# Kernel optimization log

Measured on AMD Instinct MI355X. Metric: run time of the kernel, lower is better.

## Reference

```python
import jax, jax.numpy as jnp
import numpy as np

NEG_SLOPE = 0.2
EPS = 1e-16


def gat_conv(x, src, dst, W, a_src, a_dst, bias, heads, out_ch, n_nodes):
    # x: [N, in], W: [in, heads*out_ch], a_src/a_dst: [heads, out_ch]
    h = (x @ W).reshape(n_nodes, heads, out_ch)            # [N,H,C]
    s_src = jnp.sum(h * a_src[None], axis=-1)              # [N,H]
    s_dst = jnp.sum(h * a_dst[None], axis=-1)              # [N,H]
    e = jax.nn.leaky_relu(s_src[src] + s_dst[dst], NEG_SLOPE)  # [E,H]
    # segment softmax over incoming edges of each destination node
    m = jax.ops.segment_max(e, dst, num_segments=n_nodes)  # [N,H]
    e = jnp.exp(e - m[dst])
    z = jax.ops.segment_sum(e, dst, num_segments=n_nodes)  # [N,H]
    alpha = e / (z[dst] + EPS)                             # [E,H]
    msg = h[src] * alpha[:, :, None]                       # [E,H,C]
    out = jax.ops.segment_sum(msg, dst, num_segments=n_nodes)
    return out.reshape(n_nodes, heads * out_ch) + bias


def setup_inputs() -> dict:
    key = jax.random.key(0)
    ks = jax.random.split(key, 12)
    N, E, D_IN, HID, HEADS, OUT = 100000, 1600000, 16, 128, 8, 3
    C1 = HID // HEADS  # 16 per head
    glorot = lambda k, shape: jax.random.normal(k, shape, jnp.float32) * np.sqrt(2.0 / (shape[0] + shape[-1]))
    return {
        "feature": jax.random.normal(ks[0], (N, D_IN), jnp.float32),
        "edge_index": jax.random.randint(ks[1], (2, E), 0, N, jnp.int64),
        "edge_type": jax.random.randint(ks[2], (E,), 0, 2, jnp.int64),
        "W1": glorot(ks[3], (D_IN, HEADS * C1)),
        "a_src1": glorot(ks[4], (HEADS, C1)),
        "a_dst1": glorot(ks[5], (HEADS, C1)),
        "b1": jnp.zeros((HID,), jnp.float32),
        "W2": glorot(ks[6], (HID, OUT)),
        "a_src2": glorot(ks[7], (1, OUT)),
        "a_dst2": glorot(ks[8], (1, OUT)),
        "b2": jnp.zeros((OUT,), jnp.float32),
    }


def reference(feature, edge_index, edge_type, W1, a_src1, a_dst1, b1, W2, a_src2, a_dst2, b2):
    N = feature.shape[0]
    # PyG GATConv adds self-loops by default
    loop = jnp.arange(N, dtype=edge_index.dtype)
    src = jnp.concatenate([edge_index[0], loop])
    dst = jnp.concatenate([edge_index[1], loop])
    x = gat_conv(feature, src, dst, W1, a_src1, a_dst1, b1, heads=8, out_ch=16, n_nodes=N)
    x = jax.nn.relu(x)
    # dropout is identity in eval mode
    x = gat_conv(x, src, dst, W2, a_src2, a_dst2, b2, heads=1, out_ch=3, n_nodes=N)
    return x
```

## Files before the change

kernel.cpp:

```cpp
#include <hip/hip_runtime.h>
#include <hip/hip_bf16.h>
#include <hip/hip_fp16.h>
#include <math.h>

#define NEG_SLOPE 0.2f
#define GAT_EPS 1e-16f
#define NBB_MAX 128
#define CAP   19456

__global__ __launch_bounds__(1024) void k_part(
    const int* __restrict__ ei, int E, int N, int NB,
    int* __restrict__ cnt, unsigned int* __restrict__ bp)
{
    __shared__ int hist[NBB_MAX];
    __shared__ int base[NBB_MAX];
    int t = threadIdx.x;
    int e0 = blockIdx.x * 4096;
    int srcs[4], dsts[4];
#pragma unroll
    for (int k = 0; k < 4; ++k) {
        int e = e0 + k * 1024 + t;
        if (e < E + N) {
            if (e < E) { srcs[k] = ei[e]; dsts[k] = ei[E + e]; }
            else       { srcs[k] = dsts[k] = e - E; }
        } else dsts[k] = -1;
    }
    if (t < NB) hist[t] = 0;
    __syncthreads();
#pragma unroll
    for (int k = 0; k < 4; ++k)
        if (dsts[k] >= 0) atomicAdd(&hist[dsts[k] >> 10], 1);
    __syncthreads();
    if (t < NB) {
        int c = hist[t];
        base[t] = (c > 0) ? atomicAdd(&cnt[t], c) : 0;
        hist[t] = 0;
    }
    __syncthreads();
#pragma unroll
    for (int k = 0; k < 4; ++k) {
        if (dsts[k] >= 0) {
            int b = dsts[k] >> 10;
            int r = base[b] + atomicAdd(&hist[b], 1);
            if (r < CAP)
                bp[(size_t)b * CAP + r] =
                    ((unsigned)(dsts[k] & 1023) << 17) | (unsigned)srcs[k];
        }
    }
}

__global__ __launch_bounds__(1024) void k_csrgemm(
    const unsigned int* __restrict__ bp, const int* __restrict__ cnt,
    int* __restrict__ offs, int* __restrict__ ends, int* __restrict__ csr,
    int N, int NB,
    const float* __restrict__ x, const float* __restrict__ W1,
    const float* __restrict__ a_src, const float* __restrict__ a_dst,
    __half* __restrict__ h1, float* __restrict__ s_src, float* __restrict__ s_dst)
{
    __shared__ int dcount[1024];
    __shared__ int dtmp[1024];
    __shared__ int doff[1024];
    int t = threadIdx.x;
    if (blockIdx.x >= NB) {
        int gid = (blockIdx.x - NB) * 1024 + t;
        int n = gid >> 5;
        int j4 = gid & 31;
        if (n >= N) return;
        const float4* xr = (const float4*)(x + (size_t)n * 16);
        float4 x0 = xr[0], x1 = xr[1], x2 = xr[2], x3 = xr[3];
        float xs[16] = { x0.x,x0.y,x0.z,x0.w, x1.x,x1.y,x1.z,x1.w,
                         x2.x,x2.y,x2.z,x2.w, x3.x,x3.y,x3.z,x3.w };
        const float4* W4 = (const float4*)W1;
        float4 acc = {0.f, 0.f, 0.f, 0.f};
#pragma unroll
        for (int k = 0; k < 16; ++k) {
            float4 w = W4[k * 32 + j4];
            acc.x += xs[k] * w.x;
            acc.y += xs[k] * w.y;
            acc.z += xs[k] * w.z;
            acc.w += xs[k] * w.w;
        }
        union { __half2 h2v[2]; uint2 u; } pk;
        pk.h2v[0] = __floats2half2_rn(acc.x, acc.y);
        pk.h2v[1] = __floats2half2_rn(acc.z, acc.w);
        ((uint2*)h1)[(size_t)n * 32 + j4] = pk.u;
        float4 av = ((const float4*)a_src)[j4];
        float4 dv = ((const float4*)a_dst)[j4];
        float ps = acc.x*av.x + acc.y*av.y + acc.z*av.z + acc.w*av.w;
        float pd = acc.x*dv.x + acc.y*dv.y + acc.z*dv.z + acc.w*dv.w;
        ps += __shfl_xor(ps, 1); ps += __shfl_xor(ps, 2);
        pd += __shfl_xor(pd, 1); pd += __shfl_xor(pd, 2);
        if ((j4 & 3) == 0) {
            int h = j4 >> 2;
            s_src[n * 8 + h] = ps;
            s_dst[n * 8 + h] = pd;
        }
        return;
    }
    int b = blockIdx.x;
    int rb = b * CAP;
    int m = cnt[b]; if (m > CAP) m = CAP;
    dcount[t] = 0;
    __syncthreads();
    for (int i = t; i < m; i += 1024)
        atomicAdd(&dcount[bp[rb + i] >> 17], 1);
    __syncthreads();
    int v = dcount[t];
    dtmp[t] = v;
    __syncthreads();
    for (int off = 1; off < 1024; off <<= 1) {
        int add = (t >= off) ? dtmp[t - off] : 0;
        __syncthreads();
        dtmp[t] += add;
        __syncthreads();
    }
    doff[t] = dtmp[t] - v;
    int n = b * 1024 + t;
    if (n < N) { offs[n] = rb + doff[t]; ends[n] = rb + dtmp[t]; }
    dcount[t] = 0;
    __syncthreads();
    for (int i = t; i < m; i += 1024) {
        unsigned int p = bp[rb + i];
        int dl = p >> 17;
        int r = atomicAdd(&dcount[dl], 1);
        csr[rb + doff[dl] + r] = (int)(p & 0x1FFFFu);
    }
}

__global__ __launch_bounds__(256) void k_agg1(
    const __half* __restrict__ h1, const float* __restrict__ s_src,
    const float* __restrict__ s_dst, const float* __restrict__ b1,
    const float* __restrict__ W2, const float* __restrict__ a_src2,
    const float* __restrict__ a_dst2,
    const int* __restrict__ offs, const int* __restrict__ ends,
    const int* __restrict__ csr_src,
    float4* __restrict__ h2packed, float* __restrict__ s2d, int N)
{
    int gid = blockIdx.x * 256 + threadIdx.x;
    if (gid >= N * 16) return;
    int n = gid >> 4;
    int t = gid & 15;
    int h = t & 7;
    int half = t >> 3;
    int beg = offs[n], end = ends[n];
    float sd = s_dst[n * 8 + h];

    float z = 0.f;
    float acc[16];
#pragma unroll
    for (int c = 0; c < 16; ++c) acc[c] = 0.f;

    union U { float4 f; __half2 hh[4]; };
    int i = beg + half;
    for (; i + 2 < end; i += 4) {
        int sA = csr_src[i];
        int sB = csr_src[i + 2];
        const float4* hA = (const float4*)(h1 + (size_t)sA * 128 + h * 16);
        const float4* hB = (const float4*)(h1 + (size_t)sB * 128 + h * 16);
        U a0, a1, b0, b1v;
        a0.f = hA[0]; a1.f = hA[1];
        b0.f = hB[0]; b1v.f = hB[1];
        float eA = s_src[sA * 8 + h] + sd;
        float eB = s_src[sB * 8 + h] + sd;
        eA = (eA > 0.f) ? eA : NEG_SLOPE * eA;
        eB = (eB > 0.f) ? eB : NEG_SLOPE * eB;
        float pA = __expf(eA);
        float pB = __expf(eB);
        z += pA + pB;
#pragma unroll
        for (int k = 0; k < 4; ++k) {
            float2 vA = __half22float2(a0.hh[k]);
            float2 vB = __half22float2(b0.hh[k]);
            acc[2 * k]     += pA * vA.x + pB * vB.x;
            acc[2 * k + 1] += pA * vA.y + pB * vB.y;
        }
#pragma unroll
        for (int k = 0; k < 4; ++k) {
            float2 vA = __half22float2(a1.hh[k]);
            float2 vB = __half22float2(b1v.hh[k]);
            acc[8 + 2 * k] += pA * vA.x + pB * vB.x;
            acc[9 + 2 * k] += pA * vA.y + pB * vB.y;
        }
    }
    if (i < end) {
        int sA = csr_src[i];
        const float4* hA = (const float4*)(h1 + (size_t)sA * 128 + h * 16);
        U a0, a1;
        a0.f = hA[0]; a1.f = hA[1];
        float eA = s_src[sA * 8 + h] + sd;
        eA = (eA > 0.f) ? eA : NEG_SLOPE * eA;
        float pA = __expf(eA);
        z += pA;
#pragma unroll
        for (int k = 0; k < 4; ++k) {
            float2 vA = __half22float2(a0.hh[k]);
            acc[2 * k]     += pA * vA.x;
            acc[2 * k + 1] += pA * vA.y;
        }
#pragma unroll
        for (int k = 0; k < 4; ++k) {
            float2 vA = __half22float2(a1.hh[k]);
            acc[8 + 2 * k] += pA * vA.x;
            acc[9 + 2 * k] += pA * vA.y;
        }
    }

    z += __shfl_xor(z, 8);
#pragma unroll
    for (int c = 0; c < 16; ++c) acc[c] += __shfl_xor(acc[c], 8);

    float inv = 1.f / (z + GAT_EPS);

    float r0 = 0.f, r1 = 0.f, r2 = 0.f;
    const float* bb = b1 + h * 16;
    const float* w2 = W2 + h * 16 * 3;
#pragma unroll
    for (int c = 0; c < 16; ++c) {
        float xc = fmaxf(acc[c] * inv + bb[c], 0.f);
        r0 += xc * w2[c * 3 + 0];
        r1 += xc * w2[c * 3 + 1];
        r2 += xc * w2[c * 3 + 2];
    }
#pragma unroll
    for (int m = 4; m >= 1; m >>= 1) {
        r0 += __shfl_xor(r0, m);
        r1 += __shfl_xor(r1, m);
        r2 += __shfl_xor(r2, m);
    }
    if (t == 0) {
        float ss = r0 * a_src2[0] + r1 * a_src2[1] + r2 * a_src2[2];
        float dd = r0 * a_dst2[0] + r1 * a_dst2[1] + r2 * a_dst2[2];
        float4 pk = { r0, r1, r2, ss };
        h2packed[n] = pk;
        s2d[n] = dd;
    }
}

__global__ __launch_bounds__(256) void k_agg2(
    const float4* __restrict__ h2packed, const float* __restrict__ s2d,
    const float* __restrict__ b2,
    const int* __restrict__ offs, const int* __restrict__ ends,
    const int* __restrict__ csr_src,
    float* __restrict__ out, int N)
{
    int gid = blockIdx.x * 256 + threadIdx.x;
    if (gid >= N * 8) return;
    int n = gid >> 3;
    int t = gid & 7;
    int beg = offs[n], end = ends[n];
    float sd = s2d[n];
    float z = 0.f, a0 = 0.f, a1 = 0.f, a2 = 0.f;
    for (int i = beg + t; i < end; i += 8) {
        int src = csr_src[i];
        float4 v = h2packed[src];
        float s = v.w + sd;
        s = (s > 0.f) ? s : NEG_SLOPE * s;
        float p = __expf(s);
        z += p;
        a0 += p * v.x; a1 += p * v.y; a2 += p * v.z;
    }
#pragma unroll
    for (int m = 4; m >= 1; m >>= 1) {
        z  += __shfl_xor(z, m);
        a0 += __shfl_xor(a0, m);
        a1 += __shfl_xor(a1, m);
        a2 += __shfl_xor(a2, m);
    }
    if (t == 0) {
        float inv = 1.f / (z + GAT_EPS);
        out[(size_t)n * 3 + 0] = a0 * inv + b2[0];
        out[(size_t)n * 3 + 1] = a1 * inv + b2[1];
        out[(size_t)n * 3 + 2] = a2 * inv + b2[2];
    }
}

extern "C" void kernel_launch(void* const* d_in, const int* in_sizes, int n_in,
                              void* d_out, int out_size, void* d_ws, size_t ws_size,
                              hipStream_t stream)
{
    const float* feature = (const float*)d_in[0];
    const int*   ei      = (const int*)d_in[1];
    const float* W1      = (const float*)d_in[3];
    const float* a_src1  = (const float*)d_in[4];
    const float* a_dst1  = (const float*)d_in[5];
    const float* b1      = (const float*)d_in[6];
    const float* W2      = (const float*)d_in[7];
    const float* a_src2  = (const float*)d_in[8];
    const float* a_dst2  = (const float*)d_in[9];
    const float* b2      = (const float*)d_in[10];

    const int N = in_sizes[0] / 16;
    const int E = in_sizes[1] / 2;
    const int ET = E + N;
    const int NB = (N + 1023) >> 10;

    char* p = (char*)d_ws;
    auto alloc = [&](size_t bytes) -> void* {
        void* r = (void*)p;
        p += (bytes + 255) & ~(size_t)255;
        return r;
    };
    __half* h1   = (__half*)alloc((size_t)N * 128 * 2);
    float*  s1s  = (float*)alloc((size_t)N * 8 * 4);
    float*  s1d  = (float*)alloc((size_t)N * 8 * 4);
    float4* h2pk = (float4*)alloc((size_t)N * 16);
    float*  s2dv = (float*)alloc((size_t)N * 4);
    int*    offs = (int*)alloc((size_t)N * 4);
    int*    ends = (int*)alloc((size_t)N * 4);
    int*    csr  = (int*)alloc((size_t)NB * CAP * 4);
    unsigned int* bp = (unsigned int*)alloc((size_t)NB * CAP * 4);
    int*    cnt  = (int*)alloc((size_t)NBB_MAX * 4);

    hipMemsetAsync(cnt, 0, (size_t)NB * 4, stream);

    int G2 = (ET + 4095) / 4096;
    k_part<<<G2, 1024, 0, stream>>>(ei, E, N, NB, cnt, bp);

    int G1 = (N * 32 + 1023) / 1024;
    k_csrgemm<<<NB + G1, 1024, 0, stream>>>(
        bp, cnt, offs, ends, csr, N, NB,
        feature, W1, a_src1, a_dst1, h1, s1s, s1d);

    k_agg1<<<(N * 16 + 255) / 256, 256, 0, stream>>>(
        h1, s1s, s1d, b1, W2, a_src2, a_dst2, offs, ends, csr, h2pk, s2dv, N);

    k_agg2<<<(N * 8 + 255) / 256, 256, 0, stream>>>(
        h2pk, s2dv, b2, offs, ends, csr, (float*)d_out, N);
}
```

Before: 168.8 us.

## Split layer-1 GEMM across partition and CSR kernels; unroll aggregation by four

```diff
diff --git a/kernel.cpp b/kernel.cpp
--- a/kernel.cpp
+++ b/kernel.cpp
@@ -8,13 +8,61 @@
 #define NBB_MAX 128
 #define CAP   19456
 
-__global__ __launch_bounds__(1024) void k_part(
-    const int* __restrict__ ei, int E, int N, int NB,
-    int* __restrict__ cnt, unsigned int* __restrict__ bp)
+__device__ __forceinline__ void gemm1_path(
+    int gid, int N,
+    const float* __restrict__ x, const float* __restrict__ W1,
+    const float* __restrict__ a_src, const float* __restrict__ a_dst,
+    __half* __restrict__ h1, float* __restrict__ s_src, float* __restrict__ s_dst)
+{
+    int n = gid >> 5;
+    int j4 = gid & 31;
+    if (n >= N) return;
+    const float4* xr = (const float4*)(x + (size_t)n * 16);
+    float4 x0 = xr[0], x1 = xr[1], x2 = xr[2], x3 = xr[3];
+    float xs[16] = { x0.x,x0.y,x0.z,x0.w, x1.x,x1.y,x1.z,x1.w,
+                     x2.x,x2.y,x2.z,x2.w, x3.x,x3.y,x3.z,x3.w };
+    const float4* W4 = (const float4*)W1;
+    float4 acc = {0.f, 0.f, 0.f, 0.f};
+#pragma unroll
+    for (int k = 0; k < 16; ++k) {
+        float4 w = W4[k * 32 + j4];
+        acc.x += xs[k] * w.x;
+        acc.y += xs[k] * w.y;
+        acc.z += xs[k] * w.z;
+        acc.w += xs[k] * w.w;
+    }
+    union { __half2 h2v[2]; uint2 u; } pk;
+    pk.h2v[0] = __floats2half2_rn(acc.x, acc.y);
+    pk.h2v[1] = __floats2half2_rn(acc.z, acc.w);
+    ((uint2*)h1)[(size_t)n * 32 + j4] = pk.u;
+    float4 av = ((const float4*)a_src)[j4];
+    float4 dv = ((const float4*)a_dst)[j4];
+    float ps = acc.x*av.x + acc.y*av.y + acc.z*av.z + acc.w*av.w;
+    float pd = acc.x*dv.x + acc.y*dv.y + acc.z*dv.z + acc.w*dv.w;
+    ps += __shfl_xor(ps, 1); ps += __shfl_xor(ps, 2);
+    pd += __shfl_xor(pd, 1); pd += __shfl_xor(pd, 2);
+    if ((j4 & 3) == 0) {
+        int h = j4 >> 2;
+        s_src[n * 8 + h] = ps;
+        s_dst[n * 8 + h] = pd;
+    }
+}
+
+__global__ __launch_bounds__(1024) void k_partgemm(
+    const int* __restrict__ ei, int E, int N, int NB, int G2,
+    int* __restrict__ cnt, unsigned int* __restrict__ bp,
+    const float* __restrict__ x, const float* __restrict__ W1,
+    const float* __restrict__ a_src, const float* __restrict__ a_dst,
+    __half* __restrict__ h1, float* __restrict__ s_src, float* __restrict__ s_dst)
 {
     __shared__ int hist[NBB_MAX];
     __shared__ int base[NBB_MAX];
     int t = threadIdx.x;
+    if (blockIdx.x >= G2) {
+        gemm1_path((blockIdx.x - G2) * 1024 + t, N,
+                   x, W1, a_src, a_dst, h1, s_src, s_dst);
+        return;
+    }
     int e0 = blockIdx.x * 4096;
     int srcs[4], dsts[4];
 #pragma unroll
@@ -52,7 +100,7 @@
 __global__ __launch_bounds__(1024) void k_csrgemm(
     const unsigned int* __restrict__ bp, const int* __restrict__ cnt,
     int* __restrict__ offs, int* __restrict__ ends, int* __restrict__ csr,
-    int N, int NB,
+    int N, int NB, int gemmOff,
     const float* __restrict__ x, const float* __restrict__ W1,
     const float* __restrict__ a_src, const float* __restrict__ a_dst,
     __half* __restrict__ h1, float* __restrict__ s_src, float* __restrict__ s_dst)
@@ -62,39 +110,8 @@
     __shared__ int doff[1024];
     int t = threadIdx.x;
     if (blockIdx.x >= NB) {
-        int gid = (blockIdx.x - NB) * 1024 + t;
-        int n = gid >> 5;
-        int j4 = gid & 31;
-        if (n >= N) return;
-        const float4* xr = (const float4*)(x + (size_t)n * 16);
-        float4 x0 = xr[0], x1 = xr[1], x2 = xr[2], x3 = xr[3];
-        float xs[16] = { x0.x,x0.y,x0.z,x0.w, x1.x,x1.y,x1.z,x1.w,
-                         x2.x,x2.y,x2.z,x2.w, x3.x,x3.y,x3.z,x3.w };
-        const float4* W4 = (const float4*)W1;
-        float4 acc = {0.f, 0.f, 0.f, 0.f};
-#pragma unroll
-        for (int k = 0; k < 16; ++k) {
-            float4 w = W4[k * 32 + j4];
-            acc.x += xs[k] * w.x;
-            acc.y += xs[k] * w.y;
-            acc.z += xs[k] * w.z;
-            acc.w += xs[k] * w.w;
-        }
-        union { __half2 h2v[2]; uint2 u; } pk;
-        pk.h2v[0] = __floats2half2_rn(acc.x, acc.y);
-        pk.h2v[1] = __floats2half2_rn(acc.z, acc.w);
-        ((uint2*)h1)[(size_t)n * 32 + j4] = pk.u;
-        float4 av = ((const float4*)a_src)[j4];
-        float4 dv = ((const float4*)a_dst)[j4];
-        float ps = acc.x*av.x + acc.y*av.y + acc.z*av.z + acc.w*av.w;
-        float pd = acc.x*dv.x + acc.y*dv.y + acc.z*dv.z + acc.w*dv.w;
-        ps += __shfl_xor(ps, 1); ps += __shfl_xor(ps, 2);
-        pd += __shfl_xor(pd, 1); pd += __shfl_xor(pd, 2);
-        if ((j4 & 3) == 0) {
-            int h = j4 >> 2;
-            s_src[n * 8 + h] = ps;
-            s_dst[n * 8 + h] = pd;
-        }
+        gemm1_path((blockIdx.x - NB) * 1024 + t + gemmOff, N,
+                   x, W1, a_src, a_dst, h1, s_src, s_dst);
         return;
     }
     int b = blockIdx.x;
@@ -152,6 +169,50 @@
 
     union U { float4 f; __half2 hh[4]; };
     int i = beg + half;
+    for (; i + 6 < end; i += 8) {
+        int s0 = csr_src[i];
+        int s1 = csr_src[i + 2];
+        int s2 = csr_src[i + 4];
+        int s3 = csr_src[i + 6];
+        const float4* p0 = (const float4*)(h1 + (size_t)s0 * 128 + h * 16);
+        const float4* p1 = (const float4*)(h1 + (size_t)s1 * 128 + h * 16);
+        const float4* p2 = (const float4*)(h1 + (size_t)s2 * 128 + h * 16);
+        const float4* p3 = (const float4*)(h1 + (size_t)s3 * 128 + h * 16);
+        U a0, a1, b0, b1v, c0, c1, d0, d1;
+        a0.f = p0[0]; a1.f = p0[1];
+        b0.f = p1[0]; b1v.f = p1[1];
+        c0.f = p2[0]; c1.f = p2[1];
+        d0.f = p3[0]; d1.f = p3[1];
+        float e0 = s_src[s0 * 8 + h] + sd;
+        float e1 = s_src[s1 * 8 + h] + sd;
+        float e2 = s_src[s2 * 8 + h] + sd;
+        float e3 = s_src[s3 * 8 + h] + sd;
+        e0 = (e0 > 0.f) ? e0 : NEG_SLOPE * e0;
+        e1 = (e1 > 0.f) ? e1 : NEG_SLOPE * e1;
+        e2 = (e2 > 0.f) ? e2 : NEG_SLOPE * e2;
+        e3 = (e3 > 0.f) ? e3 : NEG_SLOPE * e3;
+        float q0 = __expf(e0), q1 = __expf(e1);
+        float q2 = __expf(e2), q3 = __expf(e3);
+        z += (q0 + q1) + (q2 + q3);
+#pragma unroll
+        for (int k = 0; k < 4; ++k) {
+            float2 vA = __half22float2(a0.hh[k]);
+            float2 vB = __half22float2(b0.hh[k]);
+            float2 vC = __half22float2(c0.hh[k]);
+            float2 vD = __half22float2(d0.hh[k]);
+            acc[2 * k]     += q0 * vA.x + q1 * vB.x + q2 * vC.x + q3 * vD.x;
+            acc[2 * k + 1] += q0 * vA.y + q1 * vB.y + q2 * vC.y + q3 * vD.y;
+        }
+#pragma unroll
+        for (int k = 0; k < 4; ++k) {
+            float2 vA = __half22float2(a1.hh[k]);
+            float2 vB = __half22float2(b1v.hh[k]);
+            float2 vC = __half22float2(c1.hh[k]);
+            float2 vD = __half22float2(d1.hh[k]);
+            acc[8 + 2 * k] += q0 * vA.x + q1 * vB.x + q2 * vC.x + q3 * vD.x;
+            acc[9 + 2 * k] += q0 * vA.y + q1 * vB.y + q2 * vC.y + q3 * vD.y;
+        }
+    }
     for (; i + 2 < end; i += 4) {
         int sA = csr_src[i];
         int sB = csr_src[i + 2];
@@ -314,11 +375,16 @@
     hipMemsetAsync(cnt, 0, (size_t)NB * 4, stream);
 
     int G2 = (ET + 4095) / 4096;
-    k_part<<<G2, 1024, 0, stream>>>(ei, E, N, NB, cnt, bp);
-
     int G1 = (N * 32 + 1023) / 1024;
-    k_csrgemm<<<NB + G1, 1024, 0, stream>>>(
-        bp, cnt, offs, ends, csr, N, NB,
+    int G1A = (G1 + 1) / 2;
+    int G1B = G1 - G1A;
+
+    k_partgemm<<<G2 + G1A, 1024, 0, stream>>>(
+        ei, E, N, NB, G2, cnt, bp,
+        feature, W1, a_src1, a_dst1, h1, s1s, s1d);
+
+    k_csrgemm<<<NB + G1B, 1024, 0, stream>>>(
+        bp, cnt, offs, ends, csr, N, NB, G1A * 1024,
         feature, W1, a_src1, a_dst1, h1, s1s, s1d);
 
     k_agg1<<<(N * 16 + 255) / 256, 256, 0, stream>>>(
```

Result: no change. 169.4 us (+0.4%).
